# Kernel tuning notes

Measured on AMD Instinct MI355X. Metric: run time of the kernel, lower is better.

The kernel has to match this reference:

```python
import jax, jax.numpy as jnp
import numpy as np
from jax import lax

N, LOOKBACK, FEAT, HID, HORIZON = 8000, 12, 64, 128, 4
DENSITY = 0.002  # ~16 avg in-degree


def setup_inputs() -> dict:
    key = jax.random.key(0)
    ks = jax.random.split(key, 20)
    tspan = jnp.arange(HORIZON, dtype=jnp.float32)
    x = jax.random.normal(ks[0], (LOOKBACK, N, FEAT), dtype=jnp.float32)
    # sparse weighted adjacency: nonzero pattern with ~DENSITY fill
    mask = (jax.random.uniform(ks[1], (N, N)) < DENSITY).astype(jnp.float32)
    adj_w = mask * jax.random.uniform(ks[2], (N, N), dtype=jnp.float32)

    def lin(k, fi, fo):
        s = 1.0 / np.sqrt(fi)
        return jax.random.uniform(k, (fi, fo), minval=-s, maxval=s, dtype=jnp.float32)

    return {
        "tspan": tspan, "x": x, "adj_w": adj_w,
        # init_enc: Linear(lookback->hid), ReLU, Linear(hid->1)
        "We1": lin(ks[3], LOOKBACK, HID), "be1": jnp.zeros((HID,), jnp.float32),
        "We2": lin(ks[4], HID, 1), "be2": jnp.zeros((1,), jnp.float32),
        # f: Linear(feat->hid), ReLU, Linear(hid->feat)
        "Wf1": lin(ks[5], FEAT, HID), "bf1": jnp.zeros((HID,), jnp.float32),
        "Wf2": lin(ks[6], HID, FEAT), "bf2": jnp.zeros((FEAT,), jnp.float32),
        # SAGEConv1 (feat->hid): lin_l (aggr, with bias), lin_r (root, no bias)
        "Wl1": lin(ks[7], FEAT, HID), "bl1": jnp.zeros((HID,), jnp.float32),
        "Wr1": lin(ks[8], FEAT, HID),
        # SAGEConv2 (hid->feat)
        "Wl2": lin(ks[9], HID, FEAT), "bl2": jnp.zeros((FEAT,), jnp.float32),
        "Wr2": lin(ks[10], HID, FEAT),
    }


def reference(tspan, x, adj_w, We1, be1, We2, be2, Wf1, bf1, Wf2, bf2,
              Wl1, bl1, Wr1, Wl2, bl2, Wr2):
    # binarized adjacency from nonzero pattern (adj.nonzero() in torch)
    A = (adj_w != 0).astype(x.dtype)                      # [N, N], edge (i,j) => msg x[i] -> node j
    deg = jnp.maximum(A.sum(axis=0), 1.0)                 # in-degree per target [N]

    def sage(h, Wl, bl, Wr):
        aggr = (A.T @ h) / deg[:, None]                   # mean over in-neighbors
        return aggr @ Wl + bl + h @ Wr

    def dxdt(h):
        x_self = jax.nn.relu(h @ Wf1 + bf1) @ Wf2 + bf2
        x_neigh = sage(jax.nn.relu(sage(h, Wl1, bl1, Wr1)), Wl2, bl2, Wr2)
        return jnp.clip(x_self + x_neigh, -1000.0, 1000.0)

    # init_enc: [L,N,F] -> permute [N,F,L] -> MLP over lookback -> [N,F]
    xe = jnp.transpose(x, (1, 2, 0))                      # [N, F, L]
    x0 = (jax.nn.relu(xe @ We1 + be1) @ We2 + be2)[..., 0]  # [N, F]

    # fixed-step Euler at tspan points (torchdiffeq method='euler')
    dts = tspan[1:] - tspan[:-1]

    def step(h, dt):
        hn = h + dt * dxdt(h)
        return hn, hn

    _, xs = lax.scan(step, x0, dts)
    return jnp.concatenate([x0[None], xs], axis=0)        # [horizon, N, F]
```

## Files before the change

kernel.cpp:

```cpp
#include <hip/hip_runtime.h>

#define N_NODES 8000
#define FEAT 64
#define HID 128
#define LOOKBACK 12
#define CAP 64

__global__ __launch_bounds__(256)
void zero_cnt_kernel(int* __restrict__ cnt) {
    int g = blockIdx.x * 256 + threadIdx.x;
    if (g < N_NODES) cnt[g] = 0;
}

__global__ __launch_bounds__(256)
void build_adj_kernel(const float* __restrict__ adj, int* __restrict__ cnt,
                      int* __restrict__ lists) {
    const long NQ = (long)N_NODES * N_NODES / 4;
    const long STRIDE = 2048L * 256;
    for (long q = (long)blockIdx.x * 256 + threadIdx.x; q < NQ; q += STRIDE) {
        float4 w = *reinterpret_cast<const float4*>(adj + 4 * q);
        if (w.x != 0.0f || w.y != 0.0f || w.z != 0.0f || w.w != 0.0f) {
            int i  = (int)(q / (N_NODES / 4));
            int j0 = (int)(q % (N_NODES / 4)) * 4;
            float wv[4] = {w.x, w.y, w.z, w.w};
            #pragma unroll
            for (int c = 0; c < 4; ++c) {
                if (wv[c] != 0.0f) {
                    int j = j0 + c;
                    int p = atomicAdd(&cnt[j], 1);
                    if (p < CAP) lists[(long)j * CAP + p] = i;
                }
            }
        }
    }
}

__global__ __launch_bounds__(256)
void prep_kernel(int* __restrict__ cnt, int* __restrict__ lists,
                 float* __restrict__ degf,
                 const float* __restrict__ Wl1, const float* __restrict__ Wr1,
                 const float* __restrict__ Wl2, const float* __restrict__ Wr2,
                 float* __restrict__ Ws1, float* __restrict__ Wc2) {
    if (blockIdx.x < 2000) {
        const int wv   = threadIdx.x >> 6;
        const int lane = threadIdx.x & 63;
        const int n = blockIdx.x * 4 + wv;
        int m = cnt[n];
        if (m > CAP) m = CAP;
        int v = (lane < m) ? lists[(long)n * CAP + lane] : 0x7FFFFFFF;
        #pragma unroll
        for (int k = 2; k <= 64; k <<= 1) {
            #pragma unroll
            for (int j = k >> 1; j > 0; j >>= 1) {
                int other = __shfl_xor(v, j);
                bool keepMin = (((lane & j) == 0) == ((lane & k) == 0));
                int mn = v < other ? v : other;
                int mx = v < other ? other : v;
                v = keepMin ? mn : mx;
            }
        }
        lists[(long)n * CAP + lane] = v;
        if (lane == 0) {
            cnt[n]  = m;
            degf[n] = (float)(m > 0 ? m : 1);
        }
    } else {
        int u = (blockIdx.x - 2000) * 256 + threadIdx.x;
        if (u < 128 * 128) {
            int k = u >> 7, j = u & 127;
            Ws1[u] = (k < 64) ? Wl1[k * 128 + j] : Wr1[(k - 64) * 128 + j];
        } else if (u < 2 * 128 * 128) {
            int w = u - 128 * 128;
            int k = w >> 7, j = w & 127;
            Wc2[w] = (j < 64) ? Wl2[k * 64 + j] : Wr2[k * 64 + (j - 64)];
        }
    }
}

__global__ __launch_bounds__(256)
void init_enc_kernel(const float* __restrict__ x, const float* __restrict__ We1,
                     const float* __restrict__ be1, const float* __restrict__ We2,
                     const float* __restrict__ be2, float* __restrict__ out0) {
    __shared__ float sW1T[HID * LOOKBACK];
    __shared__ float sB1[HID];
    __shared__ float sW2[HID];
    for (int e = threadIdx.x; e < HID * LOOKBACK; e += 256) {
        int l = e / HID, h = e % HID;
        sW1T[h * LOOKBACK + l] = We1[e];
    }
    for (int e = threadIdx.x; e < HID; e += 256) { sB1[e] = be1[e]; sW2[e] = We2[e]; }
    __syncthreads();
    int g = (blockIdx.x * 256 + threadIdx.x) * 4;
    if (g >= N_NODES * FEAT) return;
    float xv[4][LOOKBACK];
    #pragma unroll
    for (int l = 0; l < LOOKBACK; ++l) {
        float4 v = *reinterpret_cast<const float4*>(x + (long)l * N_NODES * FEAT + g);
        xv[0][l] = v.x; xv[1][l] = v.y; xv[2][l] = v.z; xv[3][l] = v.w;
    }
    float b2 = be2[0];
    float acc[4] = {b2, b2, b2, b2};
    for (int h = 0; h < HID; ++h) {
        float s0 = sB1[h], s1 = s0, s2 = s0, s3 = s0;
        #pragma unroll
        for (int l = 0; l < LOOKBACK; ++l) {
            float w = sW1T[h * LOOKBACK + l];
            s0 += xv[0][l] * w; s1 += xv[1][l] * w;
            s2 += xv[2][l] * w; s3 += xv[3][l] * w;
        }
        float w2 = sW2[h];
        acc[0] += fmaxf(s0, 0.0f) * w2; acc[1] += fmaxf(s1, 0.0f) * w2;
        acc[2] += fmaxf(s2, 0.0f) * w2; acc[3] += fmaxf(s3, 0.0f) * w2;
    }
    float4 o = {acc[0], acc[1], acc[2], acc[3]};
    *reinterpret_cast<float4*>(out0 + g) = o;
}

__global__ __launch_bounds__(256)
void sageproj_kernel(const float* __restrict__ h, const int* __restrict__ lists,
                     const int* __restrict__ cnt, const float* __restrict__ degf,
                     const float* __restrict__ Ws1, const float* __restrict__ bl1,
                     const float* __restrict__ Wc2, const float* __restrict__ bl2,
                     const float* __restrict__ Wf1, const float* __restrict__ bf1,
                     const float* __restrict__ Wf2, const float* __restrict__ bf2,
                     float* __restrict__ pl, float* __restrict__ q) {
    __shared__ float v[16][132];
    __shared__ float rr[16][132];
    __shared__ float tt[16][132];
    __shared__ float xsl[16][68];
    __shared__ float wbuf[64 * 128];
    const int tid = threadIdx.x;
    const int nb = blockIdx.x * 16;
    const int ln = tid >> 4, jg = tid & 15;
    const int n = nb + ln;
    const int c0 = jg * 4;
    {
        const int m = cnt[n];
        const int* l = lists + (long)n * CAP;
        const float inv = 1.0f / degf[n];
        float4 a = {0, 0, 0, 0};
        for (int e = 0; e < m; ++e) {
            float4 b = *reinterpret_cast<const float4*>(h + (long)l[e] * FEAT + c0);
            a.x += b.x; a.y += b.y; a.z += b.z; a.w += b.w;
        }
        float4 av = {a.x * inv, a.y * inv, a.z * inv, a.w * inv};
        *reinterpret_cast<float4*>(&v[ln][c0]) = av;
        *reinterpret_cast<float4*>(&v[ln][64 + c0]) =
            *reinterpret_cast<const float4*>(h + (long)n * FEAT + c0);
    }
    {
        float4 b0 = *reinterpret_cast<const float4*>(bl1 + c0);
        float4 b1 = *reinterpret_cast<const float4*>(bl1 + 64 + c0);
        float A0[4] = {b0.x, b0.y, b0.z, b0.w};
        float A1[4] = {b1.x, b1.y, b1.z, b1.w};
        for (int kc = 0; kc < 2; ++kc) {
            __syncthreads();
            for (int e = tid; e < 2048; e += 256)
                *(reinterpret_cast<float4*>(wbuf) + e) =
                    *(reinterpret_cast<const float4*>(Ws1 + kc * 8192) + e);
            __syncthreads();
            #pragma unroll 4
            for (int k = 0; k < 64; ++k) {
                float a = v[ln][kc * 64 + k];
                float4 w0 = *reinterpret_cast<const float4*>(&wbuf[k * 128 + c0]);
                float4 w1 = *reinterpret_cast<const float4*>(&wbuf[k * 128 + 64 + c0]);
                A0[0] += a * w0.x; A0[1] += a * w0.y; A0[2] += a * w0.z; A0[3] += a * w0.w;
                A1[0] += a * w1.x; A1[1] += a * w1.y; A1[2] += a * w1.z; A1[3] += a * w1.w;
            }
        }
        float4 o0 = {fmaxf(A0[0],0.f), fmaxf(A0[1],0.f), fmaxf(A0[2],0.f), fmaxf(A0[3],0.f)};
        float4 o1 = {fmaxf(A1[0],0.f), fmaxf(A1[1],0.f), fmaxf(A1[2],0.f), fmaxf(A1[3],0.f)};
        *reinterpret_cast<float4*>(&rr[ln][c0]) = o0;
        *reinterpret_cast<float4*>(&rr[ln][64 + c0]) = o1;
    }
    {
        float4 b0 = *reinterpret_cast<const float4*>(bf1 + c0);
        float4 b1 = *reinterpret_cast<const float4*>(bf1 + 64 + c0);
        float A0[4] = {b0.x, b0.y, b0.z, b0.w};
        float A1[4] = {b1.x, b1.y, b1.z, b1.w};
        __syncthreads();
        for (int e = tid; e < 2048; e += 256)
            *(reinterpret_cast<float4*>(wbuf) + e) =
                *(reinterpret_cast<const float4*>(Wf1) + e);
        __syncthreads();
        #pragma unroll 4
        for (int k = 0; k < 64; ++k) {
            float a = v[ln][64 + k];
            float4 w0 = *reinterpret_cast<const float4*>(&wbuf[k * 128 + c0]);
            float4 w1 = *reinterpret_cast<const float4*>(&wbuf[k * 128 + 64 + c0]);
            A0[0] += a * w0.x; A0[1] += a * w0.y; A0[2] += a * w0.z; A0[3] += a * w0.w;
            A1[0] += a * w1.x; A1[1] += a * w1.y; A1[2] += a * w1.z; A1[3] += a * w1.w;
        }
        float4 o0 = {fmaxf(A0[0],0.f), fmaxf(A0[1],0.f), fmaxf(A0[2],0.f), fmaxf(A0[3],0.f)};
        float4 o1 = {fmaxf(A1[0],0.f), fmaxf(A1[1],0.f), fmaxf(A1[2],0.f), fmaxf(A1[3],0.f)};
        *reinterpret_cast<float4*>(&tt[ln][c0]) = o0;
        *reinterpret_cast<float4*>(&tt[ln][64 + c0]) = o1;
    }
    {
        float4 b0 = *reinterpret_cast<const float4*>(bf2 + c0);
        float X[4] = {b0.x, b0.y, b0.z, b0.w};
        __syncthreads();
        for (int e = tid; e < 2048; e += 256)
            *(reinterpret_cast<float4*>(wbuf) + e) =
                *(reinterpret_cast<const float4*>(Wf2) + e);
        __syncthreads();
        #pragma unroll 4
        for (int k = 0; k < 128; ++k) {
            float a = tt[ln][k];
            float4 w = *reinterpret_cast<const float4*>(&wbuf[k * 64 + c0]);
            X[0] += a * w.x; X[1] += a * w.y; X[2] += a * w.z; X[3] += a * w.w;
        }
        float4 o = {X[0], X[1], X[2], X[3]};
        *reinterpret_cast<float4*>(&xsl[ln][c0]) = o;
    }
    {
        float P0[4] = {0, 0, 0, 0};
        float P1[4] = {0, 0, 0, 0};
        for (int kc = 0; kc < 2; ++kc) {
            __syncthreads();
            for (int e = tid; e < 2048; e += 256)
                *(reinterpret_cast<float4*>(wbuf) + e) =
                    *(reinterpret_cast<const float4*>(Wc2 + kc * 8192) + e);
            __syncthreads();
            #pragma unroll 4
            for (int k = 0; k < 64; ++k) {
                float a = rr[ln][kc * 64 + k];
                float4 w0 = *reinterpret_cast<const float4*>(&wbuf[k * 128 + c0]);
                float4 w1 = *reinterpret_cast<const float4*>(&wbuf[k * 128 + 64 + c0]);
                P0[0] += a * w0.x; P0[1] += a * w0.y; P0[2] += a * w0.z; P0[3] += a * w0.w;
                P1[0] += a * w1.x; P1[1] += a * w1.y; P1[2] += a * w1.z; P1[3] += a * w1.w;
            }
        }
        float4 op = {P0[0], P0[1], P0[2], P0[3]};
        *reinterpret_cast<float4*>(pl + (long)n * FEAT + c0) = op;
        float4 bv = *reinterpret_cast<const float4*>(bl2 + c0);
        float4 oq = {P1[0] + bv.x + xsl[ln][c0 + 0],
                     P1[1] + bv.y + xsl[ln][c0 + 1],
                     P1[2] + bv.z + xsl[ln][c0 + 2],
                     P1[3] + bv.w + xsl[ln][c0 + 3]};
        *reinterpret_cast<float4*>(q + (long)n * FEAT + c0) = oq;
    }
}

__global__ __launch_bounds__(256)
void epi_kernel(const float* __restrict__ pl, const float* __restrict__ q,
                const int* __restrict__ lists, const int* __restrict__ cnt,
                const float* __restrict__ degf, const float* __restrict__ hcur,
                const float* __restrict__ tspan, int step,
                float* __restrict__ hnext) {
    const int tid = threadIdx.x;
    const int ln = tid >> 4, sub = tid & 15;
    const int n = blockIdx.x * 16 + ln;
    const int f0 = sub * 4;
    const int m = cnt[n];
    const int* l = lists + (long)n * CAP;
    const float inv = 1.0f / degf[n];
    float4 a = {0, 0, 0, 0};
    for (int e = 0; e < m; ++e) {
        float4 b = *reinterpret_cast<const float4*>(pl + (long)l[e] * FEAT + f0);
        a.x += b.x; a.y += b.y; a.z += b.z; a.w += b.w;
    }
    const float dt = tspan[step + 1] - tspan[step];
    float4 qv = *reinterpret_cast<const float4*>(q + (long)n * FEAT + f0);
    float4 hv = *reinterpret_cast<const float4*>(hcur + (long)n * FEAT + f0);
    float s0 = qv.x + a.x * inv, s1 = qv.y + a.y * inv;
    float s2 = qv.z + a.z * inv, s3 = qv.w + a.w * inv;
    s0 = fminf(fmaxf(s0, -1000.f), 1000.f); s1 = fminf(fmaxf(s1, -1000.f), 1000.f);
    s2 = fminf(fmaxf(s2, -1000.f), 1000.f); s3 = fminf(fmaxf(s3, -1000.f), 1000.f);
    float4 o = {hv.x + dt * s0, hv.y + dt * s1, hv.z + dt * s2, hv.w + dt * s3};
    *reinterpret_cast<float4*>(hnext + (long)n * FEAT + f0) = o;
}

extern "C" void kernel_launch(void* const* d_in, const int* in_sizes, int n_in,
                              void* d_out, int out_size, void* d_ws, size_t ws_size,
                              hipStream_t stream) {
    const float* tspan = (const float*)d_in[0];
    const float* x     = (const float*)d_in[1];
    const float* adj   = (const float*)d_in[2];
    const float* We1   = (const float*)d_in[3];
    const float* be1   = (const float*)d_in[4];
    const float* We2   = (const float*)d_in[5];
    const float* be2   = (const float*)d_in[6];
    const float* Wf1   = (const float*)d_in[7];
    const float* bf1   = (const float*)d_in[8];
    const float* Wf2   = (const float*)d_in[9];
    const float* bf2   = (const float*)d_in[10];
    const float* Wl1   = (const float*)d_in[11];
    const float* bl1   = (const float*)d_in[12];
    const float* Wr1   = (const float*)d_in[13];
    const float* Wl2   = (const float*)d_in[14];
    const float* bl2   = (const float*)d_in[15];
    const float* Wr2   = (const float*)d_in[16];
    float* out = (float*)d_out;

    char* ws = (char*)d_ws;
    int*   lists = (int*)  (ws + 0);
    int*   cnt   = (int*)  (ws + 2048000);
    float* degf  = (float*)(ws + 2080000);
    float* Ws1   = (float*)(ws + 2112000);
    float* Wc2   = (float*)(ws + 2177536);
    float* pl    = (float*)(ws + 2243072);
    float* q     = (float*)(ws + 4291072);

    zero_cnt_kernel<<<32, 256, 0, stream>>>(cnt);
    build_adj_kernel<<<2048, 256, 0, stream>>>(adj, cnt, lists);
    prep_kernel<<<2128, 256, 0, stream>>>(cnt, lists, degf, Wl1, Wr1, Wl2, Wr2, Ws1, Wc2);
    init_enc_kernel<<<500, 256, 0, stream>>>(x, We1, be1, We2, be2, out);

    for (int s = 0; s < 3; ++s) {
        const float* hcur  = out + (long)s       * N_NODES * FEAT;
        float*       hnext = out + (long)(s + 1) * N_NODES * FEAT;
        sageproj_kernel<<<500, 256, 0, stream>>>(hcur, lists, cnt, degf,
                                                 Ws1, bl1, Wc2, bl2,
                                                 Wf1, bf1, Wf2, bf2, pl, q);
        epi_kernel<<<500, 256, 0, stream>>>(pl, q, lists, cnt, degf, hcur, tspan, s, hnext);
    }
}
```

Before: 249.4 us.

## Fuse prep into sage kernel, merge zeroing with init encoder, prefetch weights

Folds zeroing of the count array into the init-encoder kernel. It also drops the separate prep kernel: neighbor-list sorting and degree setup move into the per-step sage projection kernel, and weights are read directly from the original matrices instead of a combined copy. Weight staging into shared memory is software-pipelined, so the next chunk is loaded into registers while the current one is used. This removes two launches and one global weight copy. The cost is redundant list sorting on every Euler step and higher register pressure from the prefetch buffer.

```diff
diff --git a/kernel.cpp b/kernel.cpp
--- a/kernel.cpp
+++ b/kernel.cpp
@@ -7,9 +7,45 @@
 #define CAP 64
 
 __global__ __launch_bounds__(256)
-void zero_cnt_kernel(int* __restrict__ cnt) {
-    int g = blockIdx.x * 256 + threadIdx.x;
-    if (g < N_NODES) cnt[g] = 0;
+void zero_init_kernel(int* __restrict__ cnt,
+                      const float* __restrict__ x,
+                      const float* __restrict__ We1, const float* __restrict__ be1,
+                      const float* __restrict__ We2, const float* __restrict__ be2,
+                      float* __restrict__ out0) {
+    __shared__ float sW1T[HID * LOOKBACK];
+    __shared__ float sB1[HID];
+    __shared__ float sW2[HID];
+    const int tid = threadIdx.x;
+    if (tid < 16) cnt[blockIdx.x * 16 + tid] = 0;
+    for (int e = tid; e < HID * LOOKBACK; e += 256) {
+        int l = e / HID, h = e % HID;
+        sW1T[h * LOOKBACK + l] = We1[e];
+    }
+    for (int e = tid; e < HID; e += 256) { sB1[e] = be1[e]; sW2[e] = We2[e]; }
+    __syncthreads();
+    int g = (blockIdx.x * 256 + tid) * 4;
+    float xv[4][LOOKBACK];
+    #pragma unroll
+    for (int l = 0; l < LOOKBACK; ++l) {
+        float4 v = *reinterpret_cast<const float4*>(x + (long)l * N_NODES * FEAT + g);
+        xv[0][l] = v.x; xv[1][l] = v.y; xv[2][l] = v.z; xv[3][l] = v.w;
+    }
+    float b2 = be2[0];
+    float acc[4] = {b2, b2, b2, b2};
+    for (int h = 0; h < HID; ++h) {
+        float s0 = sB1[h], s1 = s0, s2 = s0, s3 = s0;
+        #pragma unroll
+        for (int l = 0; l < LOOKBACK; ++l) {
+            float w = sW1T[h * LOOKBACK + l];
+            s0 += xv[0][l] * w; s1 += xv[1][l] * w;
+            s2 += xv[2][l] * w; s3 += xv[3][l] * w;
+        }
+        float w2 = sW2[h];
+        acc[0] += fmaxf(s0, 0.0f) * w2; acc[1] += fmaxf(s1, 0.0f) * w2;
+        acc[2] += fmaxf(s2, 0.0f) * w2; acc[3] += fmaxf(s3, 0.0f) * w2;
+    }
+    float4 o = {acc[0], acc[1], acc[2], acc[3]};
+    *reinterpret_cast<float4*>(out0 + g) = o;
 }
 
 __global__ __launch_bounds__(256)
@@ -36,91 +72,13 @@
 }
 
 __global__ __launch_bounds__(256)
-void prep_kernel(int* __restrict__ cnt, int* __restrict__ lists,
-                 float* __restrict__ degf,
-                 const float* __restrict__ Wl1, const float* __restrict__ Wr1,
-                 const float* __restrict__ Wl2, const float* __restrict__ Wr2,
-                 float* __restrict__ Ws1, float* __restrict__ Wc2) {
-    if (blockIdx.x < 2000) {
-        const int wv   = threadIdx.x >> 6;
-        const int lane = threadIdx.x & 63;
-        const int n = blockIdx.x * 4 + wv;
-        int m = cnt[n];
-        if (m > CAP) m = CAP;
-        int v = (lane < m) ? lists[(long)n * CAP + lane] : 0x7FFFFFFF;
-        #pragma unroll
-        for (int k = 2; k <= 64; k <<= 1) {
-            #pragma unroll
-            for (int j = k >> 1; j > 0; j >>= 1) {
-                int other = __shfl_xor(v, j);
-                bool keepMin = (((lane & j) == 0) == ((lane & k) == 0));
-                int mn = v < other ? v : other;
-                int mx = v < other ? other : v;
-                v = keepMin ? mn : mx;
-            }
-        }
-        lists[(long)n * CAP + lane] = v;
-        if (lane == 0) {
-            cnt[n]  = m;
-            degf[n] = (float)(m > 0 ? m : 1);
-        }
-    } else {
-        int u = (blockIdx.x - 2000) * 256 + threadIdx.x;
-        if (u < 128 * 128) {
-            int k = u >> 7, j = u & 127;
-            Ws1[u] = (k < 64) ? Wl1[k * 128 + j] : Wr1[(k - 64) * 128 + j];
-        } else if (u < 2 * 128 * 128) {
-            int w = u - 128 * 128;
-            int k = w >> 7, j = w & 127;
-            Wc2[w] = (j < 64) ? Wl2[k * 64 + j] : Wr2[k * 64 + (j - 64)];
-        }
-    }
-}
-
-__global__ __launch_bounds__(256)
-void init_enc_kernel(const float* __restrict__ x, const float* __restrict__ We1,
-                     const float* __restrict__ be1, const float* __restrict__ We2,
-                     const float* __restrict__ be2, float* __restrict__ out0) {
-    __shared__ float sW1T[HID * LOOKBACK];
-    __shared__ float sB1[HID];
-    __shared__ float sW2[HID];
-    for (int e = threadIdx.x; e < HID * LOOKBACK; e += 256) {
-        int l = e / HID, h = e % HID;
-        sW1T[h * LOOKBACK + l] = We1[e];
-    }
-    for (int e = threadIdx.x; e < HID; e += 256) { sB1[e] = be1[e]; sW2[e] = We2[e]; }
-    __syncthreads();
-    int g = (blockIdx.x * 256 + threadIdx.x) * 4;
-    if (g >= N_NODES * FEAT) return;
-    float xv[4][LOOKBACK];
-    #pragma unroll
-    for (int l = 0; l < LOOKBACK; ++l) {
-        float4 v = *reinterpret_cast<const float4*>(x + (long)l * N_NODES * FEAT + g);
-        xv[0][l] = v.x; xv[1][l] = v.y; xv[2][l] = v.z; xv[3][l] = v.w;
-    }
-    float b2 = be2[0];
-    float acc[4] = {b2, b2, b2, b2};
-    for (int h = 0; h < HID; ++h) {
-        float s0 = sB1[h], s1 = s0, s2 = s0, s3 = s0;
-        #pragma unroll
-        for (int l = 0; l < LOOKBACK; ++l) {
-            float w = sW1T[h * LOOKBACK + l];
-            s0 += xv[0][l] * w; s1 += xv[1][l] * w;
-            s2 += xv[2][l] * w; s3 += xv[3][l] * w;
-        }
-        float w2 = sW2[h];
-        acc[0] += fmaxf(s0, 0.0f) * w2; acc[1] += fmaxf(s1, 0.0f) * w2;
-        acc[2] += fmaxf(s2, 0.0f) * w2; acc[3] += fmaxf(s3, 0.0f) * w2;
-    }
-    float4 o = {acc[0], acc[1], acc[2], acc[3]};
-    *reinterpret_cast<float4*>(out0 + g) = o;
-}
-
-__global__ __launch_bounds__(256)
-void sageproj_kernel(const float* __restrict__ h, const int* __restrict__ lists,
-                     const int* __restrict__ cnt, const float* __restrict__ degf,
-                     const float* __restrict__ Ws1, const float* __restrict__ bl1,
-                     const float* __restrict__ Wc2, const float* __restrict__ bl2,
+void sageproj_kernel(const float* __restrict__ h, const int* __restrict__ lists_,
+                     int* __restrict__ lists, int* __restrict__ cnt,
+                     float* __restrict__ degf,
+                     const float* __restrict__ Wl1, const float* __restrict__ bl1,
+                     const float* __restrict__ Wr1,
+                     const float* __restrict__ Wl2, const float* __restrict__ bl2,
+                     const float* __restrict__ Wr2,
                      const float* __restrict__ Wf1, const float* __restrict__ bf1,
                      const float* __restrict__ Wf2, const float* __restrict__ bf2,
                      float* __restrict__ pl, float* __restrict__ q) {
@@ -131,8 +89,55 @@
     __shared__ float wbuf[64 * 128];
     const int tid = threadIdx.x;
     const int nb = blockIdx.x * 16;
+
+    float4 pf[8];
+    int next_chunk = 0;
+    auto load_chunk = [&](int c) {
+        #pragma unroll
+        for (int i = 0; i < 8; ++i) {
+            int e = tid + i * 256;
+            const float* p;
+            if      (c == 0) p = Wl1 + (long)e * 4;
+            else if (c == 1) p = Wr1 + (long)e * 4;
+            else if (c == 2) p = Wf1 + (long)e * 4;
+            else if (c == 3) p = Wf2 + (long)e * 4;
+            else {
+                int k  = (e >> 5) + ((c == 5) ? 64 : 0);
+                int jj = e & 31;
+                p = (jj < 16) ? (Wl2 + ((long)k * 16 + jj) * 4)
+                              : (Wr2 + ((long)k * 16 + jj - 16) * 4);
+            }
+            pf[i] = *reinterpret_cast<const float4*>(p);
+        }
+    };
+    load_chunk(next_chunk++);
+
+    {
+        const int wv = tid >> 6, lane = tid & 63;
+        #pragma unroll 1
+        for (int r = 0; r < 4; ++r) {
+            const int n = nb + wv * 4 + r;
+            int m = cnt[n]; if (m > CAP) m = CAP;
+            int val = (lane < m) ? lists[(long)n * CAP + lane] : 0x7FFFFFFF;
+            #pragma unroll
+            for (int k = 2; k <= 64; k <<= 1) {
+                #pragma unroll
+                for (int j = k >> 1; j > 0; j >>= 1) {
+                    int other = __shfl_xor(val, j);
+                    bool keepMin = (((lane & j) == 0) == ((lane & k) == 0));
+                    int mn = val < other ? val : other;
+                    int mx = val < other ? other : val;
+                    val = keepMin ? mn : mx;
+                }
+            }
+            lists[(long)n * CAP + lane] = val;
+            if (lane == 0) { cnt[n] = m; degf[n] = (float)(m > 0 ? m : 1); }
+        }
+    }
+    __syncthreads();
+
     const int ln = tid >> 4, jg = tid & 15;
-    const int n = nb + ln;
+    const int n  = nb + ln;
     const int c0 = jg * 4;
     {
         const int m = cnt[n];
@@ -148,17 +153,24 @@
         *reinterpret_cast<float4*>(&v[ln][64 + c0]) =
             *reinterpret_cast<const float4*>(h + (long)n * FEAT + c0);
     }
+
+    #define STAGE()                                                          \
+        do {                                                                 \
+            __syncthreads();                                                 \
+            _Pragma("unroll")                                                \
+            for (int i = 0; i < 8; ++i)                                      \
+                *(reinterpret_cast<float4*>(wbuf) + tid + i * 256) = pf[i];  \
+            if (next_chunk < 6) load_chunk(next_chunk++);                    \
+            __syncthreads();                                                 \
+        } while (0)
+
     {
         float4 b0 = *reinterpret_cast<const float4*>(bl1 + c0);
         float4 b1 = *reinterpret_cast<const float4*>(bl1 + 64 + c0);
         float A0[4] = {b0.x, b0.y, b0.z, b0.w};
         float A1[4] = {b1.x, b1.y, b1.z, b1.w};
         for (int kc = 0; kc < 2; ++kc) {
-            __syncthreads();
-            for (int e = tid; e < 2048; e += 256)
-                *(reinterpret_cast<float4*>(wbuf) + e) =
-                    *(reinterpret_cast<const float4*>(Ws1 + kc * 8192) + e);
-            __syncthreads();
+            STAGE();
             #pragma unroll 4
             for (int k = 0; k < 64; ++k) {
                 float a = v[ln][kc * 64 + k];
@@ -178,11 +190,7 @@
         float4 b1 = *reinterpret_cast<const float4*>(bf1 + 64 + c0);
         float A0[4] = {b0.x, b0.y, b0.z, b0.w};
         float A1[4] = {b1.x, b1.y, b1.z, b1.w};
-        __syncthreads();
-        for (int e = tid; e < 2048; e += 256)
-            *(reinterpret_cast<float4*>(wbuf) + e) =
-                *(reinterpret_cast<const float4*>(Wf1) + e);
-        __syncthreads();
+        STAGE();
         #pragma unroll 4
         for (int k = 0; k < 64; ++k) {
             float a = v[ln][64 + k];
@@ -199,11 +207,7 @@
     {
         float4 b0 = *reinterpret_cast<const float4*>(bf2 + c0);
         float X[4] = {b0.x, b0.y, b0.z, b0.w};
-        __syncthreads();
-        for (int e = tid; e < 2048; e += 256)
-            *(reinterpret_cast<float4*>(wbuf) + e) =
-                *(reinterpret_cast<const float4*>(Wf2) + e);
-        __syncthreads();
+        STAGE();
         #pragma unroll 4
         for (int k = 0; k < 128; ++k) {
             float a = tt[ln][k];
@@ -217,11 +221,7 @@
         float P0[4] = {0, 0, 0, 0};
         float P1[4] = {0, 0, 0, 0};
         for (int kc = 0; kc < 2; ++kc) {
-            __syncthreads();
-            for (int e = tid; e < 2048; e += 256)
-                *(reinterpret_cast<float4*>(wbuf) + e) =
-                    *(reinterpret_cast<const float4*>(Wc2 + kc * 8192) + e);
-            __syncthreads();
+            STAGE();
             #pragma unroll 4
             for (int k = 0; k < 64; ++k) {
                 float a = rr[ln][kc * 64 + k];
@@ -240,6 +240,7 @@
                      P1[3] + bv.w + xsl[ln][c0 + 3]};
         *reinterpret_cast<float4*>(q + (long)n * FEAT + c0) = oq;
     }
+    #undef STAGE
 }
 
 __global__ __launch_bounds__(256)
@@ -297,21 +298,17 @@
     int*   lists = (int*)  (ws + 0);
     int*   cnt   = (int*)  (ws + 2048000);
     float* degf  = (float*)(ws + 2080000);
-    float* Ws1   = (float*)(ws + 2112000);
-    float* Wc2   = (float*)(ws + 2177536);
-    float* pl    = (float*)(ws + 2243072);
-    float* q     = (float*)(ws + 4291072);
-
-    zero_cnt_kernel<<<32, 256, 0, stream>>>(cnt);
+    float* pl    = (float*)(ws + 2112000);
+    float* q     = (float*)(ws + 4160000);
+
+    zero_init_kernel<<<500, 256, 0, stream>>>(cnt, x, We1, be1, We2, be2, out);
     build_adj_kernel<<<2048, 256, 0, stream>>>(adj, cnt, lists);
-    prep_kernel<<<2128, 256, 0, stream>>>(cnt, lists, degf, Wl1, Wr1, Wl2, Wr2, Ws1, Wc2);
-    init_enc_kernel<<<500, 256, 0, stream>>>(x, We1, be1, We2, be2, out);
 
     for (int s = 0; s < 3; ++s) {
         const float* hcur  = out + (long)s       * N_NODES * FEAT;
         float*       hnext = out + (long)(s + 1) * N_NODES * FEAT;
-        sageproj_kernel<<<500, 256, 0, stream>>>(hcur, lists, cnt, degf,
-                                                 Ws1, bl1, Wc2, bl2,
+        sageproj_kernel<<<500, 256, 0, stream>>>(hcur, lists, lists, cnt, degf,
+                                                 Wl1, bl1, Wr1, Wl2, bl2, Wr2,
                                                  Wf1, bf1, Wf2, bf2, pl, q);
         epi_kernel<<<500, 256, 0, stream>>>(pl, q, lists, cnt, degf, hcur, tspan, s, hnext);
     }
```

Measured after the change: 302.3 us. 21.2% more time.

## Fuse adjacency build, init encoder and weight packing; move list sort into first step

Applied to the files above, without the earlier changes.

Merges the adjacency-scan kernel, the init encoder kernel and the weight-packing part of the prep kernel into one launch, dispatching on block index. The neighbour-list sort and degree computation move into the first sageproj launch, where each block sorts the lists of its own 16 nodes before gathering. This removes two kernel launches and lets the compute-bound encoder blocks run alongside the memory-bound dense adjacency scan. The cost is extra shared memory reserved for the scan blocks and a serial per-wave sort prologue in the first step.

```diff
diff --git a/kernel.cpp b/kernel.cpp
--- a/kernel.cpp
+++ b/kernel.cpp
@@ -13,63 +13,75 @@
 }
 
 __global__ __launch_bounds__(256)
-void build_adj_kernel(const float* __restrict__ adj, int* __restrict__ cnt,
-                      int* __restrict__ lists) {
-    const long NQ = (long)N_NODES * N_NODES / 4;
-    const long STRIDE = 2048L * 256;
-    for (long q = (long)blockIdx.x * 256 + threadIdx.x; q < NQ; q += STRIDE) {
-        float4 w = *reinterpret_cast<const float4*>(adj + 4 * q);
-        if (w.x != 0.0f || w.y != 0.0f || w.z != 0.0f || w.w != 0.0f) {
-            int i  = (int)(q / (N_NODES / 4));
-            int j0 = (int)(q % (N_NODES / 4)) * 4;
-            float wv[4] = {w.x, w.y, w.z, w.w};
+void bis_kernel(const float* __restrict__ adj, int* __restrict__ cnt,
+                int* __restrict__ lists,
+                const float* __restrict__ x,
+                const float* __restrict__ We1, const float* __restrict__ be1,
+                const float* __restrict__ We2, const float* __restrict__ be2,
+                float* __restrict__ out0,
+                const float* __restrict__ Wl1, const float* __restrict__ Wr1,
+                const float* __restrict__ Wl2, const float* __restrict__ Wr2,
+                float* __restrict__ Ws1, float* __restrict__ Wc2) {
+    __shared__ float sW1T[HID * LOOKBACK];
+    __shared__ float sB1[HID];
+    __shared__ float sW2[HID];
+    const int tid = threadIdx.x;
+    if (blockIdx.x < 2048) {
+        const long NQ = (long)N_NODES * N_NODES / 4;
+        const long STRIDE = 2048L * 256;
+        for (long q = (long)blockIdx.x * 256 + tid; q < NQ; q += STRIDE) {
+            float4 w = *reinterpret_cast<const float4*>(adj + 4 * q);
+            if (w.x != 0.0f || w.y != 0.0f || w.z != 0.0f || w.w != 0.0f) {
+                int i  = (int)(q / (N_NODES / 4));
+                int j0 = (int)(q % (N_NODES / 4)) * 4;
+                float wv[4] = {w.x, w.y, w.z, w.w};
+                #pragma unroll
+                for (int c = 0; c < 4; ++c) {
+                    if (wv[c] != 0.0f) {
+                        int j = j0 + c;
+                        int p = atomicAdd(&cnt[j], 1);
+                        if (p < CAP) lists[(long)j * CAP + p] = i;
+                    }
+                }
+            }
+        }
+    } else if (blockIdx.x < 2548) {
+        const int b = blockIdx.x - 2048;
+        for (int e = tid; e < HID * LOOKBACK; e += 256) {
+            int l = e / HID, h = e % HID;
+            sW1T[h * LOOKBACK + l] = We1[e];
+        }
+        for (int e = tid; e < HID; e += 256) { sB1[e] = be1[e]; sW2[e] = We2[e]; }
+        __syncthreads();
+        int g = (b * 256 + tid) * 4;
+        float xv[4][LOOKBACK];
+        #pragma unroll
+        for (int l = 0; l < LOOKBACK; ++l) {
+            float4 v = *reinterpret_cast<const float4*>(x + (long)l * N_NODES * FEAT + g);
+            xv[0][l] = v.x; xv[1][l] = v.y; xv[2][l] = v.z; xv[3][l] = v.w;
+        }
+        float b2 = be2[0];
+        float acc[4] = {b2, b2, b2, b2};
+        for (int h = 0; h < HID; ++h) {
+            float s0 = sB1[h], s1 = s0, s2 = s0, s3 = s0;
             #pragma unroll
-            for (int c = 0; c < 4; ++c) {
-                if (wv[c] != 0.0f) {
-                    int j = j0 + c;
-                    int p = atomicAdd(&cnt[j], 1);
-                    if (p < CAP) lists[(long)j * CAP + p] = i;
-                }
-            }
-        }
-    }
-}
-
-__global__ __launch_bounds__(256)
-void prep_kernel(int* __restrict__ cnt, int* __restrict__ lists,
-                 float* __restrict__ degf,
-                 const float* __restrict__ Wl1, const float* __restrict__ Wr1,
-                 const float* __restrict__ Wl2, const float* __restrict__ Wr2,
-                 float* __restrict__ Ws1, float* __restrict__ Wc2) {
-    if (blockIdx.x < 2000) {
-        const int wv   = threadIdx.x >> 6;
-        const int lane = threadIdx.x & 63;
-        const int n = blockIdx.x * 4 + wv;
-        int m = cnt[n];
-        if (m > CAP) m = CAP;
-        int v = (lane < m) ? lists[(long)n * CAP + lane] : 0x7FFFFFFF;
-        #pragma unroll
-        for (int k = 2; k <= 64; k <<= 1) {
-            #pragma unroll
-            for (int j = k >> 1; j > 0; j >>= 1) {
-                int other = __shfl_xor(v, j);
-                bool keepMin = (((lane & j) == 0) == ((lane & k) == 0));
-                int mn = v < other ? v : other;
-                int mx = v < other ? other : v;
-                v = keepMin ? mn : mx;
-            }
-        }
-        lists[(long)n * CAP + lane] = v;
-        if (lane == 0) {
-            cnt[n]  = m;
-            degf[n] = (float)(m > 0 ? m : 1);
-        }
+            for (int l = 0; l < LOOKBACK; ++l) {
+                float w = sW1T[h * LOOKBACK + l];
+                s0 += xv[0][l] * w; s1 += xv[1][l] * w;
+                s2 += xv[2][l] * w; s3 += xv[3][l] * w;
+            }
+            float w2 = sW2[h];
+            acc[0] += fmaxf(s0, 0.0f) * w2; acc[1] += fmaxf(s1, 0.0f) * w2;
+            acc[2] += fmaxf(s2, 0.0f) * w2; acc[3] += fmaxf(s3, 0.0f) * w2;
+        }
+        float4 o = {acc[0], acc[1], acc[2], acc[3]};
+        *reinterpret_cast<float4*>(out0 + g) = o;
     } else {
-        int u = (blockIdx.x - 2000) * 256 + threadIdx.x;
+        int u = (blockIdx.x - 2548) * 256 + tid;
         if (u < 128 * 128) {
             int k = u >> 7, j = u & 127;
             Ws1[u] = (k < 64) ? Wl1[k * 128 + j] : Wr1[(k - 64) * 128 + j];
-        } else if (u < 2 * 128 * 128) {
+        } else {
             int w = u - 128 * 128;
             int k = w >> 7, j = w & 127;
             Wc2[w] = (j < 64) ? Wl2[k * 64 + j] : Wr2[k * 64 + (j - 64)];
@@ -78,47 +90,9 @@
 }
 
 __global__ __launch_bounds__(256)
-void init_enc_kernel(const float* __restrict__ x, const float* __restrict__ We1,
-                     const float* __restrict__ be1, const float* __restrict__ We2,
-                     const float* __restrict__ be2, float* __restrict__ out0) {
-    __shared__ float sW1T[HID * LOOKBACK];
-    __shared__ float sB1[HID];
-    __shared__ float sW2[HID];
-    for (int e = threadIdx.x; e < HID * LOOKBACK; e += 256) {
-        int l = e / HID, h = e % HID;
-        sW1T[h * LOOKBACK + l] = We1[e];
-    }
-    for (int e = threadIdx.x; e < HID; e += 256) { sB1[e] = be1[e]; sW2[e] = We2[e]; }
-    __syncthreads();
-    int g = (blockIdx.x * 256 + threadIdx.x) * 4;
-    if (g >= N_NODES * FEAT) return;
-    float xv[4][LOOKBACK];
-    #pragma unroll
-    for (int l = 0; l < LOOKBACK; ++l) {
-        float4 v = *reinterpret_cast<const float4*>(x + (long)l * N_NODES * FEAT + g);
-        xv[0][l] = v.x; xv[1][l] = v.y; xv[2][l] = v.z; xv[3][l] = v.w;
-    }
-    float b2 = be2[0];
-    float acc[4] = {b2, b2, b2, b2};
-    for (int h = 0; h < HID; ++h) {
-        float s0 = sB1[h], s1 = s0, s2 = s0, s3 = s0;
-        #pragma unroll
-        for (int l = 0; l < LOOKBACK; ++l) {
-            float w = sW1T[h * LOOKBACK + l];
-            s0 += xv[0][l] * w; s1 += xv[1][l] * w;
-            s2 += xv[2][l] * w; s3 += xv[3][l] * w;
-        }
-        float w2 = sW2[h];
-        acc[0] += fmaxf(s0, 0.0f) * w2; acc[1] += fmaxf(s1, 0.0f) * w2;
-        acc[2] += fmaxf(s2, 0.0f) * w2; acc[3] += fmaxf(s3, 0.0f) * w2;
-    }
-    float4 o = {acc[0], acc[1], acc[2], acc[3]};
-    *reinterpret_cast<float4*>(out0 + g) = o;
-}
-
-__global__ __launch_bounds__(256)
-void sageproj_kernel(const float* __restrict__ h, const int* __restrict__ lists,
-                     const int* __restrict__ cnt, const float* __restrict__ degf,
+void sageproj_kernel(const float* __restrict__ h,
+                     int* __restrict__ lists, int* __restrict__ cnt,
+                     float* __restrict__ degf, int do_sort,
                      const float* __restrict__ Ws1, const float* __restrict__ bl1,
                      const float* __restrict__ Wc2, const float* __restrict__ bl2,
                      const float* __restrict__ Wf1, const float* __restrict__ bf1,
@@ -131,6 +105,29 @@
     __shared__ float wbuf[64 * 128];
     const int tid = threadIdx.x;
     const int nb = blockIdx.x * 16;
+    if (do_sort) {
+        const int wv = tid >> 6, lane = tid & 63;
+        #pragma unroll 1
+        for (int r = 0; r < 4; ++r) {
+            const int n = nb + wv * 4 + r;
+            int m = cnt[n]; if (m > CAP) m = CAP;
+            int val = (lane < m) ? lists[(long)n * CAP + lane] : 0x7FFFFFFF;
+            #pragma unroll
+            for (int k = 2; k <= 64; k <<= 1) {
+                #pragma unroll
+                for (int j = k >> 1; j > 0; j >>= 1) {
+                    int other = __shfl_xor(val, j);
+                    bool keepMin = (((lane & j) == 0) == ((lane & k) == 0));
+                    int mn = val < other ? val : other;
+                    int mx = val < other ? other : val;
+                    val = keepMin ? mn : mx;
+                }
+            }
+            lists[(long)n * CAP + lane] = val;
+            if (lane == 0) { cnt[n] = m; degf[n] = (float)(m > 0 ? m : 1); }
+        }
+        __syncthreads();
+    }
     const int ln = tid >> 4, jg = tid & 15;
     const int n = nb + ln;
     const int c0 = jg * 4;
@@ -303,14 +300,13 @@
     float* q     = (float*)(ws + 4291072);
 
     zero_cnt_kernel<<<32, 256, 0, stream>>>(cnt);
-    build_adj_kernel<<<2048, 256, 0, stream>>>(adj, cnt, lists);
-    prep_kernel<<<2128, 256, 0, stream>>>(cnt, lists, degf, Wl1, Wr1, Wl2, Wr2, Ws1, Wc2);
-    init_enc_kernel<<<500, 256, 0, stream>>>(x, We1, be1, We2, be2, out);
+    bis_kernel<<<2676, 256, 0, stream>>>(adj, cnt, lists, x, We1, be1, We2, be2,
+                                         out, Wl1, Wr1, Wl2, Wr2, Ws1, Wc2);
 
     for (int s = 0; s < 3; ++s) {
         const float* hcur  = out + (long)s       * N_NODES * FEAT;
         float*       hnext = out + (long)(s + 1) * N_NODES * FEAT;
-        sageproj_kernel<<<500, 256, 0, stream>>>(hcur, lists, cnt, degf,
+        sageproj_kernel<<<500, 256, 0, stream>>>(hcur, lists, cnt, degf, (s == 0) ? 1 : 0,
                                                  Ws1, bl1, Wc2, bl2,
                                                  Wf1, bf1, Wf2, bf2, pl, q);
         epi_kernel<<<500, 256, 0, stream>>>(pl, q, lists, cnt, degf, hcur, tspan, s, hnext);
```

Result: slower. 285.0 us (+14.3%).
